# Kernel tuning notes

Hardware: AMD Instinct MI355X
Metric: run time of the kernel (lower is better)

The kernel has to match this reference:

```python
import jax, jax.numpy as jnp
import numpy as np

DIN = 512      # input feature dim (din)
HEADS = 8
DHEAD = 64
DIM = HEADS * DHEAD  # 512
NTOT = 12288   # total nodes across all graphs
NBATCH = 32    # number of graphs
NMAX = 512     # padded max nodes per graph (<= pf_threshold ~562 -> softmax branch)
EPS = 1e-5


def setup_inputs() -> dict:
    key = jax.random.key(0)
    ks = jax.random.split(key, 7)
    z = jax.random.normal(ks[0], (NTOT, DIN), jnp.float32)
    src = jnp.sort(jax.random.randint(ks[1], (NTOT,), 0, NBATCH)).astype(jnp.int32)
    w_scale = 1.0 / np.sqrt(DIN)
    Wq = jax.random.normal(ks[2], (DIN, DIM), jnp.float32) * w_scale
    Wk = jax.random.normal(ks[3], (DIN, DIM), jnp.float32) * w_scale
    Wv = jax.random.normal(ks[4], (DIN, DIM), jnp.float32) * w_scale
    Wo = jax.random.normal(ks[5], (DIM, DIM), jnp.float32) * w_scale
    bo = jnp.zeros((DIM,), jnp.float32)
    ln_gamma = jnp.ones((DIN,), jnp.float32)
    ln_beta = jnp.zeros((DIN,), jnp.float32)
    return {"z": z, "src": src, "ln_gamma": ln_gamma, "ln_beta": ln_beta,
            "Wq": Wq, "Wk": Wk, "Wv": Wv, "Wo": Wo, "bo": bo,
            "n_max": NMAX, "n_batch": NBATCH}


def reference(z, src, ln_gamma, ln_beta, Wq, Wk, Wv, Wo, bo, n_max, n_batch):
    # --- LayerNorm(din) ---
    mu = jnp.mean(z, axis=-1, keepdims=True)
    var = jnp.mean(jnp.square(z - mu), axis=-1, keepdims=True)
    zn = (z - mu) * jax.lax.rsqrt(var + EPS) * ln_gamma + ln_beta

    # --- to_dense_batch(zn, src): src is sorted graph-id per node ---
    ntot = z.shape[0]
    counts = jnp.bincount(src, length=n_batch)                    # [B]
    starts = jnp.concatenate([jnp.zeros((1,), counts.dtype), jnp.cumsum(counts)[:-1]])
    pos = jnp.arange(ntot) - starts[src]                          # position within graph
    x = jnp.zeros((n_batch, n_max, DIN), zn.dtype).at[src, pos].set(zn)   # [B,N,din]
    mask = jnp.zeros((n_batch, n_max), bool).at[src, pos].set(True)       # [B,N]

    # --- q/k/v projections, split heads: b n (h d) -> b h n d ---
    def heads(t):
        return t.reshape(n_batch, n_max, HEADS, DHEAD).transpose(0, 2, 1, 3)
    q = heads(x @ Wq)
    k = heads(x @ Wk)
    v = heads(x @ Wv)

    # --- manual masked softmax attention (N <= pf_threshold branch) ---
    s = jnp.einsum('bhmd,bhnd->bhmn', q, k)
    s = jnp.where(mask[:, None, None, :], s, -jnp.inf)
    a = jax.nn.softmax(s * (DHEAD ** -0.5), axis=-1)
    o = jnp.einsum('bhmn,bhnd->bhmd', a, v)

    # --- merge heads, gather valid rows (out[mask]), output projection ---
    o = o.transpose(0, 2, 1, 3).reshape(n_batch, n_max, DIM)
    h = o[src, pos] @ Wo + bo                                     # [Ntot, DIM]
    return h
```

## Files before the change

kernel.cpp:

```cpp
#include <hip/hip_runtime.h>
#include <hip/hip_bf16.h>
#include <math.h>

#define DIN 512
#define DIM 512
#define NHEADS 8
#define DHEAD 64
#define NB 32
#define NPAD 512
#define NPTOT (NB * NPAD)

typedef __attribute__((ext_vector_type(8))) short bf16x8;
typedef __attribute__((ext_vector_type(8))) unsigned short u16x8;
typedef __attribute__((ext_vector_type(4))) float f32x4;

typedef __attribute__((address_space(3))) unsigned int lds_u32;
typedef __attribute__((address_space(1))) const unsigned int g_u32;

__device__ __forceinline__ void gll16(const unsigned short* g, unsigned short* l) {
  __builtin_amdgcn_global_load_lds((g_u32*)g, (lds_u32*)l, 16, 0, 0);
}

__device__ inline unsigned short f2bf(float x) {
  unsigned int u = __float_as_uint(x);
  unsigned int r = (u + 0x7FFFu + ((u >> 16) & 1u)) >> 16;
  return (unsigned short)r;
}

__global__ __launch_bounds__(256) void ln_kernel(const float* __restrict__ z,
                                                 const float* __restrict__ gamma,
                                                 const float* __restrict__ beta,
                                                 unsigned short* __restrict__ zn,
                                                 int ntot) {
  int wave = (blockIdx.x * blockDim.x + threadIdx.x) >> 6;
  int lane = threadIdx.x & 63;
  if (wave >= ntot) return;
  const float* row = z + (size_t)wave * DIN;
  float4 a = ((const float4*)row)[lane];
  float4 b = ((const float4*)row)[64 + lane];
  float s  = a.x + a.y + a.z + a.w + b.x + b.y + b.z + b.w;
  float sq = a.x*a.x + a.y*a.y + a.z*a.z + a.w*a.w
           + b.x*b.x + b.y*b.y + b.z*b.z + b.w*b.w;
#pragma unroll
  for (int off = 32; off; off >>= 1) {
    s  += __shfl_xor(s, off);
    sq += __shfl_xor(sq, off);
  }
  float mu  = s * (1.0f / DIN);
  float var = sq * (1.0f / DIN) - mu * mu;
  float r   = rsqrtf(var + 1e-5f);

  float4 g0 = ((const float4*)gamma)[lane];
  float4 g1 = ((const float4*)gamma)[64 + lane];
  float4 b0 = ((const float4*)beta)[lane];
  float4 b1 = ((const float4*)beta)[64 + lane];

  ushort4 o0, o1;
  o0.x = f2bf((a.x - mu) * r * g0.x + b0.x);
  o0.y = f2bf((a.y - mu) * r * g0.y + b0.y);
  o0.z = f2bf((a.z - mu) * r * g0.z + b0.z);
  o0.w = f2bf((a.w - mu) * r * g0.w + b0.w);
  o1.x = f2bf((b.x - mu) * r * g1.x + b1.x);
  o1.y = f2bf((b.y - mu) * r * g1.y + b1.y);
  o1.z = f2bf((b.z - mu) * r * g1.z + b1.z);
  o1.w = f2bf((b.w - mu) * r * g1.w + b1.w);
  ((ushort4*)(zn + (size_t)wave * DIN))[lane] = o0;
  ((ushort4*)(zn + (size_t)wave * DIN))[64 + lane] = o1;
}

__global__ __launch_bounds__(256) void mapk_starts(const int* __restrict__ src,
                                                   int* __restrict__ starts,
                                                   int* __restrict__ dstrow, int ntot) {
  if (blockIdx.x == 0 && threadIdx.x <= NB) {
    int b = threadIdx.x;
    int lo = 0, hi = ntot;
    while (lo < hi) { int mid = (lo + hi) >> 1; if (src[mid] < b) lo = mid + 1; else hi = mid; }
    starts[b] = lo;
  }
  int i = blockIdx.x * 256 + threadIdx.x;
  if (i < ntot) {
    int g = src[i];
    int lo = 0, hi = ntot;
    while (lo < hi) { int mid = (lo + hi) >> 1; if (src[mid] < g) lo = mid + 1; else hi = mid; }
    dstrow[i] = g * NPAD + (i - lo);
  }
}

__global__ __launch_bounds__(256) void wtrans4(const float* __restrict__ Wq,
                                               const float* __restrict__ Wk,
                                               const float* __restrict__ Wv,
                                               const float* __restrict__ Wo,
                                               unsigned short* __restrict__ WtQKV,
                                               unsigned short* __restrict__ WtO) {
  __shared__ float tile[32][33];
  const float* W; unsigned short* Wt;
  int z = blockIdx.z;
  if (z == 0)      { W = Wq; Wt = WtQKV; }
  else if (z == 1) { W = Wk; Wt = WtQKV + (size_t)512 * DIN; }
  else if (z == 2) { W = Wv; Wt = WtQKV + (size_t)1024 * DIN; }
  else             { W = Wo; Wt = WtO; }
  int k0 = blockIdx.x * 32;
  int n0 = blockIdx.y * 32;
  int tx = threadIdx.x & 31;
  int ty = threadIdx.x >> 5;
#pragma unroll
  for (int i = 0; i < 4; i++)
    tile[ty + i * 8][tx] = W[(size_t)(k0 + ty + i * 8) * DIM + n0 + tx];
  __syncthreads();
#pragma unroll
  for (int i = 0; i < 4; i++)
    Wt[(size_t)(n0 + ty + i * 8) * DIN + k0 + tx] = f2bf(tile[tx][ty + i * 8]);
}

__global__ __launch_bounds__(256) void vtrans_kernel(const unsigned short* __restrict__ qkvp,
                                                     unsigned short* __restrict__ vtg,
                                                     const int* __restrict__ starts) {
  __shared__ unsigned short tile[64][72];
  int p0 = blockIdx.x * 64;
  int g = p0 >> 9;
  if ((p0 & 511) >= starts[g + 1] - starts[g]) return;
  int c0 = blockIdx.y * 64;
  int chunk = (threadIdx.x & 7) * 8;
  int r = threadIdx.x >> 3;
#pragma unroll
  for (int p = 0; p < 2; p++) {
    int row = r + p * 32;
    *(u16x8*)&tile[row][chunk] = *(const u16x8*)(qkvp + (size_t)(p0 + row) * 1536 + 1024 + c0 + chunk);
  }
  __syncthreads();
#pragma unroll
  for (int p = 0; p < 2; p++) {
    int c = r + p * 32;
    u16x8 v;
#pragma unroll
    for (int i = 0; i < 8; i++) v[i] = tile[chunk + i][c];
    *(u16x8*)(vtg + (size_t)(c0 + c) * NPTOT + p0 + chunk) = v;
  }
}

template <int NCOLS, bool BIAS, bool OUT_F32, bool REMAP>
__global__ __launch_bounds__(256) void gemm_staged(const unsigned short* __restrict__ A,
                                                   const unsigned short* __restrict__ Bt,
                                                   const float* __restrict__ bias,
                                                   const int* __restrict__ remap,
                                                   unsigned short* __restrict__ Cbf,
                                                   float* __restrict__ Cf) {
  __shared__ unsigned short Al[2][128 * 32];
  __shared__ unsigned short Bl[2][128 * 32];
  int tid = threadIdx.x, lane = tid & 63, wv = tid >> 6;
  int col = lane & 15, quad = lane >> 4;
  int m0 = blockIdx.x * 128, n0 = blockIdx.y * 128;
  int msub = (wv & 1) * 64, nsub = (wv >> 1) * 64;

  int srow = lane >> 2;
  int cswz = (((lane & 3) ^ ((lane >> 3) & 3))) * 8;

  f32x4 acc[4][4];
#pragma unroll
  for (int i = 0; i < 4; i++)
#pragma unroll
    for (int j = 0; j < 4; j++) acc[i][j] = (f32x4){0.f, 0.f, 0.f, 0.f};

  auto stage = [&](int ks, int nb) {
    const unsigned short* Ab = A  + (size_t)m0 * DIN + ks * 32;
    const unsigned short* Bb = Bt + (size_t)n0 * DIN + ks * 32;
#pragma unroll
    for (int i = 0; i < 2; i++) {
      int t = wv * 2 + i;
      gll16(Ab + (size_t)(t * 16 + srow) * DIN + cswz, &Al[nb][t * 512]);
      gll16(Bb + (size_t)(t * 16 + srow) * DIN + cswz, &Bl[nb][t * 512]);
    }
  };

  stage(0, 0);
#pragma unroll 2
  for (int ks = 0; ks < 16; ks++) {
    int cur = ks & 1;
    __syncthreads();
    if (ks + 1 < 16) stage(ks + 1, 1 - cur);
    bf16x8 af[4], bfr[4];
#pragma unroll
    for (int mt = 0; mt < 4; mt++) {
      int row = msub + mt * 16 + col;
      af[mt] = *(const bf16x8*)&Al[cur][row * 32 + ((quad ^ ((row >> 1) & 3)) * 8)];
    }
#pragma unroll
    for (int nt = 0; nt < 4; nt++) {
      int row = nsub + nt * 16 + col;
      bfr[nt] = *(const bf16x8*)&Bl[cur][row * 32 + ((quad ^ ((row >> 1) & 3)) * 8)];
    }
#pragma unroll
    for (int mt = 0; mt < 4; mt++)
#pragma unroll
      for (int nt = 0; nt < 4; nt++)
        acc[mt][nt] = __builtin_amdgcn_mfma_f32_16x16x32_bf16(af[mt], bfr[nt], acc[mt][nt], 0, 0, 0);
  }

#pragma unroll
  for (int mt = 0; mt < 4; mt++) {
#pragma unroll
    for (int r = 0; r < 4; r++) {
      int mrow = m0 + msub + mt * 16 + quad * 4 + r;
      int drow = REMAP ? remap[mrow] : mrow;
#pragma unroll
      for (int nt = 0; nt < 4; nt++) {
        int ncol = n0 + nsub + nt * 16 + col;
        float v = acc[mt][nt][r] + (BIAS ? bias[ncol] : 0.f);
        size_t idx = (size_t)drow * NCOLS + ncol;
        if (OUT_F32) Cf[idx] = v; else Cbf[idx] = f2bf(v);
      }
    }
  }
}

__global__ __launch_bounds__(256, 3) void fattn_kernel(const unsigned short* __restrict__ qkvp,
                                                       const unsigned short* __restrict__ vtg,
                                                       const int* __restrict__ starts,
                                                       unsigned short* __restrict__ obuf) {
  __shared__ unsigned short Kbuf[2][64 * 64];
  __shared__ unsigned short Vbuf[2][64 * 64];
  __shared__ unsigned short Plds[4][32 * 64];
  int g = blockIdx.x, h = blockIdx.y, qt = blockIdx.z;
  int st = starts[g];
  int n  = starts[g + 1] - st;
  int q0b = qt * 128;
  if (q0b >= n) return;
  int tid = threadIdx.x, lane = tid & 63, wv = tid >> 6;
  int col = lane & 15, quad = lane >> 4;
  int q0 = q0b + wv * 32;
  bool active = q0 < n;
  int ntiles = (n + 63) >> 6;

  bf16x8 qf[2][2];
  if (active) {
#pragma unroll
    for (int a = 0; a < 2; a++) {
      int qr = q0 + a * 16 + col; if (qr >= n) qr = n - 1;
      const unsigned short* qp = qkvp + (size_t)(g * NPAD + qr) * 1536 + h * 64 + quad * 8;
      qf[a][0] = *(const bf16x8*)(qp);
      qf[a][1] = *(const bf16x8*)(qp + 32);
    }
  }

  int srow = tid >> 2;
  int sc   = (tid & 3) * 2;
  int woff0 = srow * 64 + ((sc ^ (srow & 7)) * 8);
  int woff1 = srow * 64 + (((sc + 1) ^ (srow & 7)) * 8);
  u16x8 kreg0, kreg1, vreg0, vreg1;
  auto loadregs = [&](int kt) {
    const unsigned short* kp = qkvp + (size_t)(g * NPAD + kt + srow) * 1536 + 512 + h * 64 + sc * 8;
    kreg0 = *(const u16x8*)(kp);
    kreg1 = *(const u16x8*)(kp + 8);
    const unsigned short* vp = vtg + (size_t)(h * 64 + srow) * NPTOT + g * NPAD + kt + sc * 8;
    vreg0 = *(const u16x8*)(vp);
    vreg1 = *(const u16x8*)(vp + 8);
  };
  auto writelds = [&](int b) {
    *(u16x8*)&Kbuf[b][woff0] = kreg0;
    *(u16x8*)&Kbuf[b][woff1] = kreg1;
    *(u16x8*)&Vbuf[b][woff0] = vreg0;
    *(u16x8*)&Vbuf[b][woff1] = vreg1;
  };

  bf16x8 onesv;
#pragma unroll
  for (int i = 0; i < 8; i++) onesv[i] = (short)0x3F80;

  f32x4 oa[2][4];
  f32x4 lacc[2];
#pragma unroll
  for (int a = 0; a < 2; a++) {
    lacc[a] = (f32x4){0.f, 0.f, 0.f, 0.f};
#pragma unroll
    for (int i = 0; i < 4; i++) oa[a][i] = (f32x4){0.f, 0.f, 0.f, 0.f};
  }

  loadregs(0);
  writelds(0);
  __syncthreads();

  for (int t = 0; t < ntiles; t++) {
    int cur = t & 1;
    if (t + 1 < ntiles) loadregs((t + 1) * 64);
    if (active) {
      f32x4 s[2][4];
#pragma unroll
      for (int a = 0; a < 2; a++)
#pragma unroll
        for (int j = 0; j < 4; j++) s[a][j] = (f32x4){0.f, 0.f, 0.f, 0.f};
#pragma unroll
      for (int j = 0; j < 4; j++) {
        int R = j * 16 + col;
        bf16x8 kf0 = *(const bf16x8*)&Kbuf[cur][R * 64 + ((quad ^ (R & 7)) * 8)];
        bf16x8 kf1 = *(const bf16x8*)&Kbuf[cur][R * 64 + (((4 + quad) ^ (R & 7)) * 8)];
        s[0][j] = __builtin_amdgcn_mfma_f32_16x16x32_bf16(qf[0][0], kf0, s[0][j], 0, 0, 0);
        s[0][j] = __builtin_amdgcn_mfma_f32_16x16x32_bf16(qf[0][1], kf1, s[0][j], 0, 0, 0);
        s[1][j] = __builtin_amdgcn_mfma_f32_16x16x32_bf16(qf[1][0], kf0, s[1][j], 0, 0, 0);
        s[1][j] = __builtin_amdgcn_mfma_f32_16x16x32_bf16(qf[1][1], kf1, s[1][j], 0, 0, 0);
      }
      int kt = t * 64;
#pragma unroll
      for (int j = 0; j < 4; j++) {
        bool valid = (kt + j * 16 + col) < n;
#pragma unroll
        for (int a = 0; a < 2; a++)
#pragma unroll
          for (int r = 0; r < 4; r++)
            s[a][j][r] = valid ? __expf(s[a][j][r] * 0.125f) : 0.f;
      }
#pragma unroll
      for (int a = 0; a < 2; a++)
#pragma unroll
        for (int r = 0; r < 4; r++) {
          int R = a * 16 + quad * 4 + r;
#pragma unroll
          for (int j = 0; j < 4; j++) {
            int chunk = j * 2 + (col >> 3);
            Plds[wv][R * 64 + ((chunk ^ (R & 7)) * 8) + (col & 7)] = f2bf(s[a][j][r]);
          }
        }
      __builtin_amdgcn_fence(__ATOMIC_ACQ_REL, "workgroup");
      bf16x8 pf[2][2];
#pragma unroll
      for (int a = 0; a < 2; a++) {
        int R = a * 16 + col;
        pf[a][0] = *(const bf16x8*)&Plds[wv][R * 64 + ((quad ^ (col & 7)) * 8)];
        pf[a][1] = *(const bf16x8*)&Plds[wv][R * 64 + (((4 + quad) ^ (col & 7)) * 8)];
      }
#pragma unroll
      for (int dt = 0; dt < 4; dt++) {
        int R = dt * 16 + col;
        bf16x8 vf0 = *(const bf16x8*)&Vbuf[cur][R * 64 + ((quad ^ (R & 7)) * 8)];
        bf16x8 vf1 = *(const bf16x8*)&Vbuf[cur][R * 64 + (((4 + quad) ^ (R & 7)) * 8)];
        oa[0][dt] = __builtin_amdgcn_mfma_f32_16x16x32_bf16(pf[0][0], vf0, oa[0][dt], 0, 0, 0);
        oa[0][dt] = __builtin_amdgcn_mfma_f32_16x16x32_bf16(pf[0][1], vf1, oa[0][dt], 0, 0, 0);
        oa[1][dt] = __builtin_amdgcn_mfma_f32_16x16x32_bf16(pf[1][0], vf0, oa[1][dt], 0, 0, 0);
        oa[1][dt] = __builtin_amdgcn_mfma_f32_16x16x32_bf16(pf[1][1], vf1, oa[1][dt], 0, 0, 0);
      }
      lacc[0] = __builtin_amdgcn_mfma_f32_16x16x32_bf16(pf[0][0], onesv, lacc[0], 0, 0, 0);
      lacc[0] = __builtin_amdgcn_mfma_f32_16x16x32_bf16(pf[0][1], onesv, lacc[0], 0, 0, 0);
      lacc[1] = __builtin_amdgcn_mfma_f32_16x16x32_bf16(pf[1][0], onesv, lacc[1], 0, 0, 0);
      lacc[1] = __builtin_amdgcn_mfma_f32_16x16x32_bf16(pf[1][1], onesv, lacc[1], 0, 0, 0);
    }
    if (t + 1 < ntiles) writelds(1 - cur);
    __syncthreads();
  }

  if (active) {
#pragma unroll
    for (int a = 0; a < 2; a++)
#pragma unroll
      for (int r = 0; r < 4; r++) {
        int q = q0 + a * 16 + quad * 4 + r;
        if (q < n) {
          float inv = 1.0f / lacc[a][r];
          unsigned short* op = obuf + (size_t)(st + q) * DIM + h * 64 + col;
          op[0]  = f2bf(oa[a][0][r] * inv);
          op[16] = f2bf(oa[a][1][r] * inv);
          op[32] = f2bf(oa[a][2][r] * inv);
          op[48] = f2bf(oa[a][3][r] * inv);
        }
      }
  }
}

extern "C" void kernel_launch(void* const* d_in, const int* in_sizes, int n_in,
                              void* d_out, int out_size, void* d_ws, size_t ws_size,
                              hipStream_t stream) {
  const float* z     = (const float*)d_in[0];
  const int*   src   = (const int*)d_in[1];
  const float* gamma = (const float*)d_in[2];
  const float* beta  = (const float*)d_in[3];
  const float* Wq    = (const float*)d_in[4];
  const float* Wk    = (const float*)d_in[5];
  const float* Wv    = (const float*)d_in[6];
  const float* Wo    = (const float*)d_in[7];
  const float* bo    = (const float*)d_in[8];
  int ntot = in_sizes[0] / DIN;
  float* out = (float*)d_out;

  char* ws = (char*)d_ws;
  size_t off = 0;
  unsigned short* zn    = (unsigned short*)(ws + off); off += (size_t)ntot * DIN * 2;
  unsigned short* qkvp  = (unsigned short*)(ws + off); off += (size_t)NPTOT * 1536 * 2;
  unsigned short* obuf  = (unsigned short*)(ws + off); off += (size_t)ntot * DIM * 2;
  unsigned short* vtg   = (unsigned short*)(ws + off); off += (size_t)DIM * NPTOT * 2;
  unsigned short* WtQKV = (unsigned short*)(ws + off); off += (size_t)1536 * DIN * 2;
  unsigned short* WtO   = (unsigned short*)(ws + off); off += (size_t)DIM * DIN * 2;
  int* starts           = (int*)(ws + off);            off += 64 * 4;
  int* dstrow           = (int*)(ws + off);

  wtrans4<<<dim3(16, 16, 4), 256, 0, stream>>>(Wq, Wk, Wv, Wo, WtQKV, WtO);
  ln_kernel<<<ntot / 4, 256, 0, stream>>>(z, gamma, beta, zn, ntot);
  mapk_starts<<<(ntot + 255) / 256, 256, 0, stream>>>(src, starts, dstrow, ntot);

  gemm_staged<1536, false, false, true>
      <<<dim3(ntot / 128, 12), 256, 0, stream>>>(zn, WtQKV, nullptr, dstrow, qkvp, nullptr);

  vtrans_kernel<<<dim3(NPTOT / 64, 8), 256, 0, stream>>>(qkvp, vtg, starts);

  fattn_kernel<<<dim3(NB, NHEADS, 4), 256, 0, stream>>>(qkvp, vtg, starts, obuf);

  gemm_staged<512, true, true, false>
      <<<dim3(ntot / 128, 4), 256, 0, stream>>>(obuf, WtO, bo, nullptr, nullptr, out);
}
```

Before: 185.1 us.

## Fuse prep kernels, drop V transpose pass, stage GEMM epilogue through LDS

LayerNorm, graph-start/remap computation and weight transposition are merged into one launch. The separate V-transpose kernel and its global buffer are removed; the attention kernel now reads V rows directly from the QKV buffer and transposes them into swizzled LDS while staging. The bf16 GEMM epilogue writes its tile to LDS and then stores coalesced 16-byte rows. The query row clamp for rows past n is also dropped. Together these cut kernel launches and a full global round trip for V, at the cost of scalar scattered LDS writes in the attention staging loop.

```diff
diff --git a/kernel.cpp b/kernel.cpp
--- a/kernel.cpp
+++ b/kernel.cpp
@@ -27,114 +27,91 @@
   return (unsigned short)r;
 }
 
-__global__ __launch_bounds__(256) void ln_kernel(const float* __restrict__ z,
-                                                 const float* __restrict__ gamma,
-                                                 const float* __restrict__ beta,
-                                                 unsigned short* __restrict__ zn,
-                                                 int ntot) {
-  int wave = (blockIdx.x * blockDim.x + threadIdx.x) >> 6;
-  int lane = threadIdx.x & 63;
-  if (wave >= ntot) return;
-  const float* row = z + (size_t)wave * DIN;
-  float4 a = ((const float4*)row)[lane];
-  float4 b = ((const float4*)row)[64 + lane];
-  float s  = a.x + a.y + a.z + a.w + b.x + b.y + b.z + b.w;
-  float sq = a.x*a.x + a.y*a.y + a.z*a.z + a.w*a.w
-           + b.x*b.x + b.y*b.y + b.z*b.z + b.w*b.w;
-#pragma unroll
-  for (int off = 32; off; off >>= 1) {
-    s  += __shfl_xor(s, off);
-    sq += __shfl_xor(sq, off);
-  }
-  float mu  = s * (1.0f / DIN);
-  float var = sq * (1.0f / DIN) - mu * mu;
-  float r   = rsqrtf(var + 1e-5f);
-
-  float4 g0 = ((const float4*)gamma)[lane];
-  float4 g1 = ((const float4*)gamma)[64 + lane];
-  float4 b0 = ((const float4*)beta)[lane];
-  float4 b1 = ((const float4*)beta)[64 + lane];
-
-  ushort4 o0, o1;
-  o0.x = f2bf((a.x - mu) * r * g0.x + b0.x);
-  o0.y = f2bf((a.y - mu) * r * g0.y + b0.y);
-  o0.z = f2bf((a.z - mu) * r * g0.z + b0.z);
-  o0.w = f2bf((a.w - mu) * r * g0.w + b0.w);
-  o1.x = f2bf((b.x - mu) * r * g1.x + b1.x);
-  o1.y = f2bf((b.y - mu) * r * g1.y + b1.y);
-  o1.z = f2bf((b.z - mu) * r * g1.z + b1.z);
-  o1.w = f2bf((b.w - mu) * r * g1.w + b1.w);
-  ((ushort4*)(zn + (size_t)wave * DIN))[lane] = o0;
-  ((ushort4*)(zn + (size_t)wave * DIN))[64 + lane] = o1;
-}
-
-__global__ __launch_bounds__(256) void mapk_starts(const int* __restrict__ src,
+__global__ __launch_bounds__(256) void prep_kernel(const float* __restrict__ z,
+                                                   const float* __restrict__ gamma,
+                                                   const float* __restrict__ beta,
+                                                   const int* __restrict__ src,
+                                                   const float* __restrict__ Wq,
+                                                   const float* __restrict__ Wk,
+                                                   const float* __restrict__ Wv,
+                                                   const float* __restrict__ Wo,
+                                                   unsigned short* __restrict__ zn,
                                                    int* __restrict__ starts,
-                                                   int* __restrict__ dstrow, int ntot) {
-  if (blockIdx.x == 0 && threadIdx.x <= NB) {
-    int b = threadIdx.x;
-    int lo = 0, hi = ntot;
-    while (lo < hi) { int mid = (lo + hi) >> 1; if (src[mid] < b) lo = mid + 1; else hi = mid; }
-    starts[b] = lo;
-  }
-  int i = blockIdx.x * 256 + threadIdx.x;
-  if (i < ntot) {
-    int g = src[i];
-    int lo = 0, hi = ntot;
-    while (lo < hi) { int mid = (lo + hi) >> 1; if (src[mid] < g) lo = mid + 1; else hi = mid; }
-    dstrow[i] = g * NPAD + (i - lo);
-  }
-}
-
-__global__ __launch_bounds__(256) void wtrans4(const float* __restrict__ Wq,
-                                               const float* __restrict__ Wk,
-                                               const float* __restrict__ Wv,
-                                               const float* __restrict__ Wo,
-                                               unsigned short* __restrict__ WtQKV,
-                                               unsigned short* __restrict__ WtO) {
+                                                   int* __restrict__ dstrow,
+                                                   unsigned short* __restrict__ WtQKV,
+                                                   unsigned short* __restrict__ WtO,
+                                                   int ntot) {
   __shared__ float tile[32][33];
-  const float* W; unsigned short* Wt;
-  int z = blockIdx.z;
-  if (z == 0)      { W = Wq; Wt = WtQKV; }
-  else if (z == 1) { W = Wk; Wt = WtQKV + (size_t)512 * DIN; }
-  else if (z == 2) { W = Wv; Wt = WtQKV + (size_t)1024 * DIN; }
-  else             { W = Wo; Wt = WtO; }
-  int k0 = blockIdx.x * 32;
-  int n0 = blockIdx.y * 32;
-  int tx = threadIdx.x & 31;
-  int ty = threadIdx.x >> 5;
-#pragma unroll
-  for (int i = 0; i < 4; i++)
-    tile[ty + i * 8][tx] = W[(size_t)(k0 + ty + i * 8) * DIM + n0 + tx];
-  __syncthreads();
-#pragma unroll
-  for (int i = 0; i < 4; i++)
-    Wt[(size_t)(n0 + ty + i * 8) * DIN + k0 + tx] = f2bf(tile[tx][ty + i * 8]);
-}
-
-__global__ __launch_bounds__(256) void vtrans_kernel(const unsigned short* __restrict__ qkvp,
-                                                     unsigned short* __restrict__ vtg,
-                                                     const int* __restrict__ starts) {
-  __shared__ unsigned short tile[64][72];
-  int p0 = blockIdx.x * 64;
-  int g = p0 >> 9;
-  if ((p0 & 511) >= starts[g + 1] - starts[g]) return;
-  int c0 = blockIdx.y * 64;
-  int chunk = (threadIdx.x & 7) * 8;
-  int r = threadIdx.x >> 3;
-#pragma unroll
-  for (int p = 0; p < 2; p++) {
-    int row = r + p * 32;
-    *(u16x8*)&tile[row][chunk] = *(const u16x8*)(qkvp + (size_t)(p0 + row) * 1536 + 1024 + c0 + chunk);
-  }
-  __syncthreads();
-#pragma unroll
-  for (int p = 0; p < 2; p++) {
-    int c = r + p * 32;
-    u16x8 v;
-#pragma unroll
-    for (int i = 0; i < 8; i++) v[i] = tile[chunk + i][c];
-    *(u16x8*)(vtg + (size_t)(c0 + c) * NPTOT + p0 + chunk) = v;
+  int b = blockIdx.x;
+  int nln = ntot >> 2;
+  int nmap = (ntot + 255) >> 8;
+  if (b < nln) {
+    int wave = b * 4 + (threadIdx.x >> 6);
+    int lane = threadIdx.x & 63;
+    const float* row = z + (size_t)wave * DIN;
+    float4 a = ((const float4*)row)[lane];
+    float4 bb = ((const float4*)row)[64 + lane];
+    float s  = a.x + a.y + a.z + a.w + bb.x + bb.y + bb.z + bb.w;
+    float sq = a.x*a.x + a.y*a.y + a.z*a.z + a.w*a.w
+             + bb.x*bb.x + bb.y*bb.y + bb.z*bb.z + bb.w*bb.w;
+#pragma unroll
+    for (int off = 32; off; off >>= 1) {
+      s  += __shfl_xor(s, off);
+      sq += __shfl_xor(sq, off);
+    }
+    float mu  = s * (1.0f / DIN);
+    float var = sq * (1.0f / DIN) - mu * mu;
+    float r   = rsqrtf(var + 1e-5f);
+    float4 g0 = ((const float4*)gamma)[lane];
+    float4 g1 = ((const float4*)gamma)[64 + lane];
+    float4 b0 = ((const float4*)beta)[lane];
+    float4 b1 = ((const float4*)beta)[64 + lane];
+    ushort4 o0, o1;
+    o0.x = f2bf((a.x - mu) * r * g0.x + b0.x);
+    o0.y = f2bf((a.y - mu) * r * g0.y + b0.y);
+    o0.z = f2bf((a.z - mu) * r * g0.z + b0.z);
+    o0.w = f2bf((a.w - mu) * r * g0.w + b0.w);
+    o1.x = f2bf((bb.x - mu) * r * g1.x + b1.x);
+    o1.y = f2bf((bb.y - mu) * r * g1.y + b1.y);
+    o1.z = f2bf((bb.z - mu) * r * g1.z + b1.z);
+    o1.w = f2bf((bb.w - mu) * r * g1.w + b1.w);
+    ((ushort4*)(zn + (size_t)wave * DIN))[lane] = o0;
+    ((ushort4*)(zn + (size_t)wave * DIN))[64 + lane] = o1;
+  } else if (b < nln + nmap) {
+    int bid = b - nln;
+    if (bid == 0 && threadIdx.x <= NB) {
+      int gg = threadIdx.x;
+      int lo = 0, hi = ntot;
+      while (lo < hi) { int mid = (lo + hi) >> 1; if (src[mid] < gg) lo = mid + 1; else hi = mid; }
+      starts[gg] = lo;
+    }
+    int i = bid * 256 + threadIdx.x;
+    if (i < ntot) {
+      int gg = src[i];
+      int lo = 0, hi = ntot;
+      while (lo < hi) { int mid = (lo + hi) >> 1; if (src[mid] < gg) lo = mid + 1; else hi = mid; }
+      dstrow[i] = gg * NPAD + (i - lo);
+    }
+  } else {
+    int idx = b - nln - nmap;
+    int zz = idx >> 8;
+    int rem = idx & 255;
+    const float* W; unsigned short* Wt;
+    if (zz == 0)      { W = Wq; Wt = WtQKV; }
+    else if (zz == 1) { W = Wk; Wt = WtQKV + (size_t)512 * DIN; }
+    else if (zz == 2) { W = Wv; Wt = WtQKV + (size_t)1024 * DIN; }
+    else              { W = Wo; Wt = WtO; }
+    int k0 = (rem & 15) * 32;
+    int n0 = (rem >> 4) * 32;
+    int tx = threadIdx.x & 31;
+    int ty = threadIdx.x >> 5;
+#pragma unroll
+    for (int i = 0; i < 4; i++)
+      tile[ty + i * 8][tx] = W[(size_t)(k0 + ty + i * 8) * DIM + n0 + tx];
+    __syncthreads();
+#pragma unroll
+    for (int i = 0; i < 4; i++)
+      Wt[(size_t)(n0 + ty + i * 8) * DIN + k0 + tx] = f2bf(tile[tx][ty + i * 8]);
   }
 }
 
@@ -145,8 +122,7 @@
                                                    const int* __restrict__ remap,
                                                    unsigned short* __restrict__ Cbf,
                                                    float* __restrict__ Cf) {
-  __shared__ unsigned short Al[2][128 * 32];
-  __shared__ unsigned short Bl[2][128 * 32];
+  __shared__ unsigned short smem[16384];
   int tid = threadIdx.x, lane = tid & 63, wv = tid >> 6;
   int col = lane & 15, quad = lane >> 4;
   int m0 = blockIdx.x * 128, n0 = blockIdx.y * 128;
@@ -167,8 +143,8 @@
 #pragma unroll
     for (int i = 0; i < 2; i++) {
       int t = wv * 2 + i;
-      gll16(Ab + (size_t)(t * 16 + srow) * DIN + cswz, &Al[nb][t * 512]);
-      gll16(Bb + (size_t)(t * 16 + srow) * DIN + cswz, &Bl[nb][t * 512]);
+      gll16(Ab + (size_t)(t * 16 + srow) * DIN + cswz, smem + nb * 4096 + t * 512);
+      gll16(Bb + (size_t)(t * 16 + srow) * DIN + cswz, smem + 8192 + nb * 4096 + t * 512);
     }
   };
 
@@ -182,12 +158,12 @@
 #pragma unroll
     for (int mt = 0; mt < 4; mt++) {
       int row = msub + mt * 16 + col;
-      af[mt] = *(const bf16x8*)&Al[cur][row * 32 + ((quad ^ ((row >> 1) & 3)) * 8)];
+      af[mt] = *(const bf16x8*)&smem[cur * 4096 + row * 32 + ((quad ^ ((row >> 1) & 3)) * 8)];
     }
 #pragma unroll
     for (int nt = 0; nt < 4; nt++) {
       int row = nsub + nt * 16 + col;
-      bfr[nt] = *(const bf16x8*)&Bl[cur][row * 32 + ((quad ^ ((row >> 1) & 3)) * 8)];
+      bfr[nt] = *(const bf16x8*)&smem[8192 + cur * 4096 + row * 32 + ((quad ^ ((row >> 1) & 3)) * 8)];
     }
 #pragma unroll
     for (int mt = 0; mt < 4; mt++)
@@ -196,25 +172,47 @@
         acc[mt][nt] = __builtin_amdgcn_mfma_f32_16x16x32_bf16(af[mt], bfr[nt], acc[mt][nt], 0, 0, 0);
   }
 
-#pragma unroll
-  for (int mt = 0; mt < 4; mt++) {
-#pragma unroll
-    for (int r = 0; r < 4; r++) {
-      int mrow = m0 + msub + mt * 16 + quad * 4 + r;
-      int drow = REMAP ? remap[mrow] : mrow;
-#pragma unroll
-      for (int nt = 0; nt < 4; nt++) {
-        int ncol = n0 + nsub + nt * 16 + col;
-        float v = acc[mt][nt][r] + (BIAS ? bias[ncol] : 0.f);
-        size_t idx = (size_t)drow * NCOLS + ncol;
-        if (OUT_F32) Cf[idx] = v; else Cbf[idx] = f2bf(v);
+  if (!OUT_F32) {
+    __syncthreads();
+#pragma unroll
+    for (int mt = 0; mt < 4; mt++)
+#pragma unroll
+      for (int r = 0; r < 4; r++) {
+        int row = msub + mt * 16 + quad * 4 + r;
+#pragma unroll
+        for (int nt = 0; nt < 4; nt++) {
+          int c = nsub + nt * 16 + col;
+          float v = acc[mt][nt][r] + (BIAS ? bias[n0 + c] : 0.f);
+          smem[row * 128 + (((c >> 3) ^ (quad << 1)) * 8) + (c & 7)] = f2bf(v);
+        }
+      }
+    __syncthreads();
+#pragma unroll
+    for (int pass = 0; pass < 8; pass++) {
+      int row = pass * 16 + (tid >> 4);
+      int sw  = ((row >> 2) & 3) << 1;
+      int ch  = tid & 15;
+      u16x8 vv = *(const u16x8*)&smem[row * 128 + ((ch ^ sw) * 8)];
+      int drow = REMAP ? remap[m0 + row] : (m0 + row);
+      *(u16x8*)(Cbf + (size_t)drow * NCOLS + n0 + ch * 8) = vv;
+    }
+  } else {
+#pragma unroll
+    for (int mt = 0; mt < 4; mt++) {
+#pragma unroll
+      for (int r = 0; r < 4; r++) {
+        int mrow = m0 + msub + mt * 16 + quad * 4 + r;
+#pragma unroll
+        for (int nt = 0; nt < 4; nt++) {
+          int ncol = n0 + nsub + nt * 16 + col;
+          Cf[(size_t)mrow * NCOLS + ncol] = acc[mt][nt][r] + (BIAS ? bias[ncol] : 0.f);
+        }
       }
     }
   }
 }
 
 __global__ __launch_bounds__(256, 3) void fattn_kernel(const unsigned short* __restrict__ qkvp,
-                                                       const unsigned short* __restrict__ vtg,
                                                        const int* __restrict__ starts,
                                                        unsigned short* __restrict__ obuf) {
   __shared__ unsigned short Kbuf[2][64 * 64];
@@ -235,8 +233,7 @@
   if (active) {
 #pragma unroll
     for (int a = 0; a < 2; a++) {
-      int qr = q0 + a * 16 + col; if (qr >= n) qr = n - 1;
-      const unsigned short* qp = qkvp + (size_t)(g * NPAD + qr) * 1536 + h * 64 + quad * 8;
+      const unsigned short* qp = qkvp + (size_t)(g * NPAD + q0 + a * 16 + col) * 1536 + h * 64 + quad * 8;
       qf[a][0] = *(const bf16x8*)(qp);
       qf[a][1] = *(const bf16x8*)(qp + 32);
     }
@@ -251,15 +248,19 @@
     const unsigned short* kp = qkvp + (size_t)(g * NPAD + kt + srow) * 1536 + 512 + h * 64 + sc * 8;
     kreg0 = *(const u16x8*)(kp);
     kreg1 = *(const u16x8*)(kp + 8);
-    const unsigned short* vp = vtg + (size_t)(h * 64 + srow) * NPTOT + g * NPAD + kt + sc * 8;
-    vreg0 = *(const u16x8*)(vp);
-    vreg1 = *(const u16x8*)(vp + 8);
+    vreg0 = *(const u16x8*)(kp + 512);
+    vreg1 = *(const u16x8*)(kp + 520);
   };
-  auto writelds = [&](int b) {
-    *(u16x8*)&Kbuf[b][woff0] = kreg0;
-    *(u16x8*)&Kbuf[b][woff1] = kreg1;
-    *(u16x8*)&Vbuf[b][woff0] = vreg0;
-    *(u16x8*)&Vbuf[b][woff1] = vreg1;
+  auto writelds = [&](int bsel) {
+    *(u16x8*)&Kbuf[bsel][woff0] = kreg0;
+    *(u16x8*)&Kbuf[bsel][woff1] = kreg1;
+#pragma unroll
+    for (int i = 0; i < 8; i++) {
+      int c0 = sc * 8 + i;
+      int c1 = sc * 8 + 8 + i;
+      Vbuf[bsel][c0 * 64 + (((srow >> 3) ^ ((c0 >> 4) << 1) ^ (c0 & 7)) * 8) + (srow & 7)] = vreg0[i];
+      Vbuf[bsel][c1 * 64 + (((srow >> 3) ^ ((c1 >> 4) << 1) ^ (c1 & 7)) * 8) + (srow & 7)] = vreg1[i];
+    }
   };
 
   bf16x8 onesv;
@@ -330,8 +331,9 @@
 #pragma unroll
       for (int dt = 0; dt < 4; dt++) {
         int R = dt * 16 + col;
-        bf16x8 vf0 = *(const bf16x8*)&Vbuf[cur][R * 64 + ((quad ^ (R & 7)) * 8)];
-        bf16x8 vf1 = *(const bf16x8*)&Vbuf[cur][R * 64 + (((4 + quad) ^ (R & 7)) * 8)];
+        int gR = ((R >> 4) << 1) ^ (R & 7);
+        bf16x8 vf0 = *(const bf16x8*)&Vbuf[cur][R * 64 + ((quad ^ gR) * 8)];
+        bf16x8 vf1 = *(const bf16x8*)&Vbuf[cur][R * 64 + (((quad + 4) ^ gR) * 8)];
         oa[0][dt] = __builtin_amdgcn_mfma_f32_16x16x32_bf16(pf[0][0], vf0, oa[0][dt], 0, 0, 0);
         oa[0][dt] = __builtin_amdgcn_mfma_f32_16x16x32_bf16(pf[0][1], vf1, oa[0][dt], 0, 0, 0);
         oa[1][dt] = __builtin_amdgcn_mfma_f32_16x16x32_bf16(pf[1][0], vf0, oa[1][dt], 0, 0, 0);
@@ -384,22 +386,20 @@
   unsigned short* zn    = (unsigned short*)(ws + off); off += (size_t)ntot * DIN * 2;
   unsigned short* qkvp  = (unsigned short*)(ws + off); off += (size_t)NPTOT * 1536 * 2;
   unsigned short* obuf  = (unsigned short*)(ws + off); off += (size_t)ntot * DIM * 2;
-  unsigned short* vtg   = (unsigned short*)(ws + off); off += (size_t)DIM * NPTOT * 2;
   unsigned short* WtQKV = (unsigned short*)(ws + off); off += (size_t)1536 * DIN * 2;
   unsigned short* WtO   = (unsigned short*)(ws + off); off += (size_t)DIM * DIN * 2;
   int* starts           = (int*)(ws + off);            off += 64 * 4;
   int* dstrow           = (int*)(ws + off);
 
-  wtrans4<<<dim3(16, 16, 4), 256, 0, stream>>>(Wq, Wk, Wv, Wo, WtQKV, WtO);
-  ln_kernel<<<ntot / 4, 256, 0, stream>>>(z, gamma, beta, zn, ntot);
-  mapk_starts<<<(ntot + 255) / 256, 256, 0, stream>>>(src, starts, dstrow, ntot);
+  int nln = ntot >> 2;
+  int nmap = (ntot + 255) >> 8;
+  prep_kernel<<<nln + nmap + 1024, 256, 0, stream>>>(z, gamma, beta, src, Wq, Wk, Wv, Wo,
+                                                     zn, starts, dstrow, WtQKV, WtO, ntot);
 
   gemm_staged<1536, false, false, true>
       <<<dim3(ntot / 128, 12), 256, 0, stream>>>(zn, WtQKV, nullptr, dstrow, qkvp, nullptr);
 
-  vtrans_kernel<<<dim3(NPTOT / 64, 8), 256, 0, stream>>>(qkvp, vtg, starts);
-
-  fattn_kernel<<<dim3(NB, NHEADS, 4), 256, 0, stream>>>(qkvp, vtg, starts, obuf);
+  fattn_kernel<<<dim3(NB, NHEADS, 4), 256, 0, stream>>>(qkvp, starts, obuf);
 
   gemm_staged<512, true, true, false>
       <<<dim3(ntot / 128, 4), 256, 0, stream>>>(obuf, WtO, bo, nullptr, nullptr, out);
```

New measurement: 171.1 us. -7.6%, faster.
